# Kernel tuning notes

Measured on AMD Instinct MI355X. Metric: run time of the kernel, lower is better.

## Reference

```python
import jax, jax.numpy as jnp
import numpy as np

N = 4096          # num_nodes == batch (every node sampled once)
D_EMB = 512       # n_embd (temporal encoder width)
D_GNN = 256       # gnn_embd
H = 2             # num_heads (hardcoded in GraphAttentionLayer default)
D_HEAD = D_GNN // H
FUS = D_EMB + D_GNN
EDGE_P = 32.0 / N # avg degree ~ max_neighbors
ALPHA = 0.2
NEG_INF = -9e15


def layer_norm(x, g, b, eps=1e-5):
    m = jnp.mean(x, axis=-1, keepdims=True)
    v = jnp.var(x, axis=-1, keepdims=True)
    return (x - m) / jnp.sqrt(v + eps) * g + b


def setup_inputs() -> dict:
    key = jax.random.key(0)
    ks = jax.random.split(key, 12)
    s = lambda fan: 1.0 / np.sqrt(fan)
    h_temporal = jax.random.normal(ks[0], (N, D_EMB), jnp.float32)
    node_indices = jnp.arange(N, dtype=jnp.int32)
    adj = (jax.random.uniform(ks[1], (N, N)) < EDGE_P).astype(jnp.float32)
    adj = jnp.maximum(adj, jnp.eye(N, dtype=jnp.float32))  # self-loops
    W_proj = jax.random.normal(ks[2], (D_EMB, D_GNN), jnp.float32) * s(D_EMB)
    b_proj = jnp.zeros((D_GNN,), jnp.float32)
    W_gat = jax.random.normal(ks[3], (H, D_GNN, D_HEAD), jnp.float32) * s(D_GNN)
    a_gat = jax.random.normal(ks[4], (H, 2 * D_HEAD), jnp.float32) * s(2 * D_HEAD)
    node_emb = jax.random.normal(ks[5], (N, D_GNN), jnp.float32) * 0.02
    ln_g = jnp.ones((D_GNN,), jnp.float32)
    ln_b = jnp.zeros((D_GNN,), jnp.float32)
    ln2_g = jnp.ones((FUS,), jnp.float32)
    ln2_b = jnp.zeros((FUS,), jnp.float32)
    W1 = jax.random.normal(ks[6], (FUS, FUS // 2), jnp.float32) * s(FUS)
    b1 = jnp.zeros((FUS // 2,), jnp.float32)
    W2 = jax.random.normal(ks[7], (FUS // 2, 1), jnp.float32) * s(FUS // 2)
    b2 = jnp.zeros((1,), jnp.float32)
    return dict(h_temporal=h_temporal, node_indices=node_indices, adj=adj,
                W_proj=W_proj, b_proj=b_proj, W_gat=W_gat, a_gat=a_gat,
                node_emb=node_emb, ln_g=ln_g, ln_b=ln_b,
                ln2_g=ln2_g, ln2_b=ln2_b, W1=W1, b1=b1, W2=W2, b2=b2)


def reference(h_temporal, node_indices, adj, W_proj, b_proj, W_gat, a_gat,
              node_emb, ln_g, ln_b, ln2_g, ln2_b, W1, b1, W2, b2):
    # gnn_proj
    h_gnn_in = h_temporal @ W_proj + b_proj                     # (B, D_GNN)
    # scatter-mean of batch features onto graph nodes (torch.unique + index_add_)
    counts = jax.ops.segment_sum(jnp.ones((h_gnn_in.shape[0],), h_gnn_in.dtype),
                                 node_indices, num_segments=N)
    sums = jax.ops.segment_sum(h_gnn_in, node_indices, num_segments=N)
    uniq_feats = sums / jnp.clip(counts, 1.0)[:, None]
    # nodes present in batch use averaged temporal feats, others keep learned embedding
    sub_feats = jnp.where((counts > 0)[:, None], uniq_feats, node_emb)  # (N, D_GNN)
    # multi-head GAT: e[h,i,j] = leakyrelu(a1_h . Wh_i + a2_h . Wh_j)
    Wh = jnp.einsum('ni,hid->hnd', sub_feats, W_gat)            # (H, N, d)
    f_src = jnp.einsum('hnd,hd->hn', Wh, a_gat[:, :D_HEAD])     # query half
    f_dst = jnp.einsum('hnd,hd->hn', Wh, a_gat[:, D_HEAD:])     # key half
    e = jax.nn.leaky_relu(f_src[:, :, None] + f_dst[:, None, :], ALPHA)  # (H,N,N)
    e = jnp.where(adj[None] > 0, e, NEG_INF)
    att = jax.nn.softmax(e, axis=-1)                            # softmax over neighbors j
    hp = jnp.einsum('hnm,hmd->hnd', att, Wh)                    # (H, N, d)
    hp = jnp.transpose(hp, (1, 0, 2)).reshape(N, D_GNN)         # concat heads
    hp = jax.nn.elu(hp)                                         # concat=True
    sub_out = layer_norm(hp, ln_g, ln_b)
    h_graph = sub_out[node_indices]                             # gather back to batch
    # fusion head
    hc = jnp.concatenate([h_temporal, h_graph], axis=-1)        # (B, FUS)
    z = layer_norm(hc, ln2_g, ln2_b)
    z = jax.nn.gelu(z @ W1 + b1, approximate=False)
    out = z @ W2 + b2                                           # (B, 1)
    return out
```

## Files before the change

kernel.cpp:

```cpp
#include <hip/hip_runtime.h>
#include <hip/hip_bf16.h>
#include <math.h>

#define N_NODES 4096
#define D_EMB   512
#define D_GNN   256
#define D_HEAD  128
#define FUS     768
#define D_HID   384
#define MAX_NBR 512

typedef unsigned short u16;
typedef __attribute__((ext_vector_type(4))) float f4;
typedef __attribute__((ext_vector_type(4))) int   i4;
typedef __attribute__((address_space(3))) u16 lds_u16;
typedef __attribute__((address_space(1))) const u16 g_u16;

__device__ __forceinline__ u16 bfh(float x) {
    __hip_bfloat16 b = __float2bfloat16(x);
    return *(u16*)&b;
}
__device__ __forceinline__ float bff(u16 u) {
    __hip_bfloat16 b = *(__hip_bfloat16*)&u;
    return __bfloat162float(b);
}

#define MFMA(acc, a, b) \
    asm volatile("v_mfma_f32_16x16x32_bf16 %0, %1, %2, %0" : "+v"(acc) : "v"(a), "v"(b))

__device__ __forceinline__ float block_reduce(float v, float* red, bool is_max) {
    #pragma unroll
    for (int o = 32; o; o >>= 1)
        v = is_max ? fmaxf(v, __shfl_down(v, o)) : v + __shfl_down(v, o);
    const int wid = threadIdx.x >> 6;
    if ((threadIdx.x & 63) == 0) red[wid] = v;
    __syncthreads();
    float r;
    if (is_max) r = fmaxf(fmaxf(red[0], red[1]), fmaxf(red[2], red[3]));
    else        r = red[0] + red[1] + red[2] + red[3];
    __syncthreads();
    return r;
}

__global__ __launch_bounds__(256) void split_rm(const float* __restrict__ X,
                                                u16* __restrict__ H, u16* __restrict__ L,
                                                int n4) {
    const int i = blockIdx.x * 256 + threadIdx.x;
    if (i >= n4) return;
    const float4 v = ((const float4*)X)[i];
    ushort4 h, l;
    h.x = bfh(v.x); l.x = bfh(v.x - bff(h.x));
    h.y = bfh(v.y); l.y = bfh(v.y - bff(h.y));
    h.z = bfh(v.z); l.z = bfh(v.z - bff(h.z));
    h.w = bfh(v.w); l.w = bfh(v.w - bff(h.w));
    ((ushort4*)H)[i] = h;
    ((ushort4*)L)[i] = l;
}

__device__ __forceinline__ void split_t_body(const float* __restrict__ W,
                                             u16* __restrict__ Th, u16* __restrict__ Tl,
                                             int K, int Nn, int bx, int by,
                                             float (*tile)[33]) {
    const int k0 = by * 32, n0 = bx * 32;
    const int lx = threadIdx.x & 31, ly = threadIdx.x >> 5;
    #pragma unroll
    for (int r = ly; r < 32; r += 8)
        tile[r][lx] = W[(size_t)(k0 + r) * Nn + n0 + lx];
    __syncthreads();
    #pragma unroll
    for (int r = ly; r < 32; r += 8) {
        const float v = tile[lx][r];
        const u16 h = bfh(v);
        const size_t o = (size_t)(n0 + r) * K + k0 + lx;
        Th[o] = h;
        Tl[o] = bfh(v - bff(h));
    }
}

__global__ __launch_bounds__(256) void prep_w(const float* __restrict__ Wproj,
                                              const float* __restrict__ W1,
                                              const float* __restrict__ Wgat,
                                              u16* __restrict__ WpTh, u16* __restrict__ WpTl,
                                              u16* __restrict__ W1Th, u16* __restrict__ W1Tl,
                                              u16* __restrict__ bTh,  u16* __restrict__ bTl) {
    __shared__ float tile[32][33];
    const int b = blockIdx.x;
    if (b < 128) {
        split_t_body(Wproj, WpTh, WpTl, D_EMB, D_GNN, b & 7, b >> 3, tile);
    } else if (b < 416) {
        const int i = b - 128;
        split_t_body(W1, W1Th, W1Tl, FUS, D_HID, i % 12, i / 12, tile);
    } else {
        const int i = b - 416;
        const int n = threadIdx.x;
        const int h = n >> 7, d = n & 127;
        const float v = Wgat[(size_t)h * D_GNN * D_HEAD + (size_t)i * D_HEAD + d];
        const u16 hh = bfh(v);
        bTh[(size_t)n * D_GNN + i] = hh;
        bTl[(size_t)n * D_GNN + i] = bfh(v - bff(hh));
    }
}

template<int SPLIT>
__global__ __launch_bounds__(256) void mgemm(const u16* __restrict__ Ah, const u16* __restrict__ Al,
                                             const u16* __restrict__ Bh, const u16* __restrict__ Bl,
                                             float* __restrict__ C,
                                             int M, int Nn, int K) {
    __shared__ u16 lds[2][4][4096];
    const int t = threadIdx.x, w = t >> 6, l = t & 63;
    const int m0 = blockIdx.y * 64, n0 = blockIdx.x * 64;
    const int nk_per = (K >> 6) / SPLIT;
    const int kt0 = blockIdx.z * nk_per;
    float* Cz = C + (size_t)blockIdx.z * M * Nn;
    const u16* pAh = Ah + (size_t)(m0 + (t >> 3)) * K + (t & 7) * 8;
    const u16* pAl = Al + (size_t)(m0 + (t >> 3)) * K + (t & 7) * 8;
    const u16* pBh = Bh + (size_t)(n0 + (t >> 3)) * K + (t & 7) * 8;
    const u16* pBl = Bl + (size_t)(n0 + (t >> 3)) * K + (t & 7) * 8;
    const int w512 = w * 512;
    const int K32 = K * 32;

#define STG(c, koff) do { \
    __builtin_amdgcn_global_load_lds((g_u16*)(pAh + (koff)),       (lds_u16*)&lds[c][0][w512],        16, 0, 0); \
    __builtin_amdgcn_global_load_lds((g_u16*)(pAh + (koff) + K32), (lds_u16*)&lds[c][0][w512 + 2048], 16, 0, 0); \
    __builtin_amdgcn_global_load_lds((g_u16*)(pAl + (koff)),       (lds_u16*)&lds[c][1][w512],        16, 0, 0); \
    __builtin_amdgcn_global_load_lds((g_u16*)(pAl + (koff) + K32), (lds_u16*)&lds[c][1][w512 + 2048], 16, 0, 0); \
    __builtin_amdgcn_global_load_lds((g_u16*)(pBh + (koff)),       (lds_u16*)&lds[c][2][w512],        16, 0, 0); \
    __builtin_amdgcn_global_load_lds((g_u16*)(pBh + (koff) + K32), (lds_u16*)&lds[c][2][w512 + 2048], 16, 0, 0); \
    __builtin_amdgcn_global_load_lds((g_u16*)(pBl + (koff)),       (lds_u16*)&lds[c][3][w512],        16, 0, 0); \
    __builtin_amdgcn_global_load_lds((g_u16*)(pBl + (koff) + K32), (lds_u16*)&lds[c][3][w512 + 2048], 16, 0, 0); \
} while (0)

    const int wm = w >> 1, wn = w & 1;
    const int lr = l & 15, lk = (l >> 4) << 3;
    int aoff[2][2], boff[2][2];
    #pragma unroll
    for (int i = 0; i < 2; ++i)
        #pragma unroll
        for (int ks = 0; ks < 2; ++ks) {
            aoff[i][ks] = (wm * 32 + i * 16 + lr) * 64 + ks * 32 + lk;
            boff[i][ks] = (wn * 32 + i * 16 + lr) * 64 + ks * 32 + lk;
        }

    f4 acc[2][2] = {};
    int cur = 0;
    STG(0, kt0 * 64);
    __syncthreads();
    for (int kt = kt0; kt < kt0 + nk_per; ++kt) {
        if (kt + 1 < kt0 + nk_per) STG(cur ^ 1, (kt + 1) * 64);
        const u16* LAh = lds[cur][0];
        const u16* LAl = lds[cur][1];
        const u16* LBh = lds[cur][2];
        const u16* LBl = lds[cur][3];
        i4 ah[2][2], al_[2][2], bh[2][2], bl_[2][2];
        #pragma unroll
        for (int i = 0; i < 2; ++i)
            #pragma unroll
            for (int ks = 0; ks < 2; ++ks) {
                ah[i][ks]  = *(const i4*)&LAh[aoff[i][ks]];
                al_[i][ks] = *(const i4*)&LAl[aoff[i][ks]];
                bh[i][ks]  = *(const i4*)&LBh[boff[i][ks]];
                bl_[i][ks] = *(const i4*)&LBl[boff[i][ks]];
            }
        #pragma unroll
        for (int i = 0; i < 2; ++i)
            #pragma unroll
            for (int j = 0; j < 2; ++j)
                #pragma unroll
                for (int ks = 0; ks < 2; ++ks) {
                    MFMA(acc[i][j], ah[i][ks],  bh[j][ks]);
                    MFMA(acc[i][j], ah[i][ks],  bl_[j][ks]);
                    MFMA(acc[i][j], al_[i][ks], bh[j][ks]);
                }
        __syncthreads();
        cur ^= 1;
    }
    asm volatile("s_nop 7\n\ts_nop 7\n\ts_nop 7");
    #pragma unroll
    for (int i = 0; i < 2; ++i)
        #pragma unroll
        for (int j = 0; j < 2; ++j) {
            const int col = n0 + wn * 32 + j * 16 + lr;
            #pragma unroll
            for (int r = 0; r < 4; ++r) {
                const int row = m0 + wm * 32 + i * 16 + (l >> 4) * 4 + r;
                Cz[(size_t)row * Nn + col] = acc[i][j][r];
            }
        }
#undef STG
}

template<bool GELU, bool HASB>
__global__ __launch_bounds__(256) void redk(const float* __restrict__ A,
                                            const float* __restrict__ B,
                                            const float* __restrict__ bias,
                                            float* __restrict__ C,
                                            int n4, int nb4) {
    const int i = blockIdx.x * 256 + threadIdx.x;
    if (i >= n4) return;
    const float4 a = ((const float4*)A)[i];
    const float4 b = ((const float4*)B)[i];
    float4 c = make_float4(a.x + b.x, a.y + b.y, a.z + b.z, a.w + b.w);
    if (HASB) {
        const float4 bv = ((const float4*)bias)[i % nb4];
        c.x += bv.x; c.y += bv.y; c.z += bv.z; c.w += bv.w;
    }
    if (GELU) {
        c.x = 0.5f * c.x * (1.f + erff(c.x * 0.70710678118654752f));
        c.y = 0.5f * c.y * (1.f + erff(c.y * 0.70710678118654752f));
        c.z = 0.5f * c.z * (1.f + erff(c.z * 0.70710678118654752f));
        c.w = 0.5f * c.w * (1.f + erff(c.w * 0.70710678118654752f));
    }
    ((float4*)C)[i] = c;
}

__global__ __launch_bounds__(256) void scatter_add(const float* __restrict__ hgnn,
                                                   const int* __restrict__ nidx,
                                                   float* __restrict__ sums,
                                                   float* __restrict__ counts) {
    const int b = blockIdx.x, t = threadIdx.x;
    const int g = nidx[b];
    atomicAdd(&sums[(size_t)g * D_GNN + t], hgnn[(size_t)b * D_GNN + t]);
    if (t == 0) atomicAdd(&counts[g], 1.0f);
}

__global__ __launch_bounds__(256) void combine(const float* __restrict__ sums,
                                               const float* __restrict__ counts,
                                               const float* __restrict__ nemb,
                                               u16* __restrict__ subh,
                                               u16* __restrict__ subl) {
    const int n = blockIdx.x, t = threadIdx.x;
    const float c = counts[n];
    const size_t o = (size_t)n * D_GNN + t;
    const float v = (c > 0.f) ? sums[o] / fmaxf(c, 1.f) : nemb[o];
    const u16 h = bfh(v);
    subh[o] = h;
    subl[o] = bfh(v - bff(h));
}

__global__ __launch_bounds__(256) void fsd(const float* __restrict__ Wh,
                                           const float* __restrict__ agat,
                                           float* __restrict__ fsrc,
                                           float* __restrict__ fdst) {
    const int n = blockIdx.x * 4 + (threadIdx.x >> 6);
    const int l = threadIdx.x & 63;
    const float* row = Wh + (size_t)n * D_GNN;
    const float x0 = row[l],       x1 = row[l + 64];
    const float y0 = row[128 + l], y1 = row[192 + l];
    float s0 = x0 * agat[l]       + x1 * agat[l + 64];
    float s1 = x0 * agat[128 + l] + x1 * agat[192 + l];
    float s2 = y0 * agat[256 + l] + y1 * agat[320 + l];
    float s3 = y0 * agat[384 + l] + y1 * agat[448 + l];
    #pragma unroll
    for (int o = 32; o; o >>= 1) {
        s0 += __shfl_down(s0, o); s1 += __shfl_down(s1, o);
        s2 += __shfl_down(s2, o); s3 += __shfl_down(s3, o);
    }
    if (l == 0) {
        fsrc[n] = s0;            fdst[n] = s1;
        fsrc[N_NODES + n] = s2;  fdst[N_NODES + n] = s3;
    }
}

__global__ __launch_bounds__(256) void gat_attn(const float* __restrict__ adj,
                                                const float* __restrict__ Wh,
                                                const float* __restrict__ fsrc,
                                                const float* __restrict__ fdst,
                                                const float* __restrict__ lng,
                                                const float* __restrict__ lnb,
                                                float* __restrict__ subout) {
    const int i = blockIdx.x, t = threadIdx.x;
    const int lane = t & 63, wid = t >> 6;
    __shared__ int   s_nbr[MAX_NBR];
    __shared__ int   s_wsum[4];
    __shared__ float s_att[2][MAX_NBR];
    __shared__ float s_red[4];
    __shared__ float s_inv[2];

    const float4* arow4 = (const float4*)(adj + (size_t)i * N_NODES) + t * 4;
    const float4 c0 = arow4[0], c1 = arow4[1], c2 = arow4[2], c3 = arow4[3];
    float v[16];
    *(float4*)&v[0]  = c0; *(float4*)&v[4]  = c1;
    *(float4*)&v[8]  = c2; *(float4*)&v[12] = c3;
    int mask = 0;
    #pragma unroll
    for (int k = 0; k < 16; ++k) mask |= (v[k] > 0.f) ? (1 << k) : 0;
    const int cnt_t = __popc(mask);

    int pre = cnt_t;
    #pragma unroll
    for (int o = 1; o < 64; o <<= 1) {
        const int u = __shfl_up(pre, o);
        if (lane >= o) pre += u;
    }
    if (lane == 63) s_wsum[wid] = pre;
    __syncthreads();
    int base = 0;
    for (int w = 0; w < wid; ++w) base += s_wsum[w];
    const int total = s_wsum[0] + s_wsum[1] + s_wsum[2] + s_wsum[3];
    int off = base + pre - cnt_t;
    #pragma unroll
    for (int k = 0; k < 16; ++k)
        if ((mask >> k) & 1) {
            if (off < MAX_NBR) s_nbr[off] = t * 16 + k;
            ++off;
        }
    __syncthreads();
    const int cnt = min(total, MAX_NBR);

    for (int h = 0; h < 2; ++h) {
        const float fs = fsrc[h * N_NODES + i];
        const float* fd = fdst + h * N_NODES;
        float lm = -1e30f;
        for (int idx = t; idx < cnt; idx += 256) {
            float e = fs + fd[s_nbr[idx]];
            e = e > 0.f ? e : 0.2f * e;
            s_att[h][idx] = e;
            lm = fmaxf(lm, e);
        }
        const float m = block_reduce(lm, s_red, true);
        float ls = 0.f;
        for (int idx = t; idx < cnt; idx += 256) {
            const float p = expf(s_att[h][idx] - m);
            s_att[h][idx] = p;
            ls += p;
        }
        const float s = block_reduce(ls, s_red, false);
        if (t == 0) s_inv[h] = 1.f / s;
    }
    __syncthreads();

    const int h = t >> 7, d = t & 127;
    float acc = 0.f;
    for (int j = 0; j < cnt; ++j)
        acc += s_att[h][j] * Wh[(size_t)s_nbr[j] * D_GNN + h * D_HEAD + d];
    acc *= s_inv[h];
    const float vv = acc > 0.f ? acc : expm1f(acc);
    const float sum  = block_reduce(vv, s_red, false);
    const float sq   = block_reduce(vv * vv, s_red, false);
    const float mean = sum * (1.f / 256.f);
    const float var  = sq * (1.f / 256.f) - mean * mean;
    const float rstd = rsqrtf(var + 1e-5f);
    subout[(size_t)i * D_GNN + t] = (vv - mean) * rstd * lng[t] + lnb[t];
}

__global__ __launch_bounds__(256) void fuse_ln(const float* __restrict__ ht,
                                               const float* __restrict__ subout,
                                               const int* __restrict__ nidx,
                                               const float* __restrict__ g,
                                               const float* __restrict__ b,
                                               u16* __restrict__ znh,
                                               u16* __restrict__ znl) {
    const int row = blockIdx.x, t = threadIdx.x;
    __shared__ float s_red[4];
    const int gidx = nidx[row];
    const float x0 = ht[(size_t)row * D_EMB + t];
    const float x1 = ht[(size_t)row * D_EMB + 256 + t];
    const float x2 = subout[(size_t)gidx * D_GNN + t];
    const float sum = block_reduce(x0 + x1 + x2, s_red, false);
    const float sq  = block_reduce(x0 * x0 + x1 * x1 + x2 * x2, s_red, false);
    const float mean = sum * (1.f / 768.f);
    const float var  = sq * (1.f / 768.f) - mean * mean;
    const float rstd = rsqrtf(var + 1e-5f);
    const size_t base = (size_t)row * FUS;
    const float z0 = (x0 - mean) * rstd * g[t]       + b[t];
    const float z1 = (x1 - mean) * rstd * g[256 + t] + b[256 + t];
    const float z2 = (x2 - mean) * rstd * g[512 + t] + b[512 + t];
    u16 h;
    h = bfh(z0); znh[base + t]       = h; znl[base + t]       = bfh(z0 - bff(h));
    h = bfh(z1); znh[base + 256 + t] = h; znl[base + 256 + t] = bfh(z1 - bff(h));
    h = bfh(z2); znh[base + 512 + t] = h; znl[base + 512 + t] = bfh(z2 - bff(h));
}

__global__ __launch_bounds__(256) void outk(const float* __restrict__ z1,
                                            const float* __restrict__ W2,
                                            const float* __restrict__ b2,
                                            float* __restrict__ out) {
    const int row = blockIdx.x * 4 + (threadIdx.x >> 6);
    const int l = threadIdx.x & 63;
    float acc = 0.f;
    for (int c = l; c < D_HID; c += 64)
        acc += z1[(size_t)row * D_HID + c] * W2[c];
    #pragma unroll
    for (int o = 32; o; o >>= 1) acc += __shfl_down(acc, o);
    if (l == 0) out[row] = acc + b2[0];
}

extern "C" void kernel_launch(void* const* d_in, const int* in_sizes, int n_in,
                              void* d_out, int out_size, void* d_ws, size_t ws_size,
                              hipStream_t stream) {
    const float* ht    = (const float*)d_in[0];
    const int*   nidx  = (const int*)  d_in[1];
    const float* adj   = (const float*)d_in[2];
    const float* Wproj = (const float*)d_in[3];
    const float* bproj = (const float*)d_in[4];
    const float* Wgat  = (const float*)d_in[5];
    const float* agat  = (const float*)d_in[6];
    const float* nemb  = (const float*)d_in[7];
    const float* lng   = (const float*)d_in[8];
    const float* lnb   = (const float*)d_in[9];
    const float* ln2g  = (const float*)d_in[10];
    const float* ln2b  = (const float*)d_in[11];
    const float* W1    = (const float*)d_in[12];
    const float* b1    = (const float*)d_in[13];
    const float* W2    = (const float*)d_in[14];
    const float* b2    = (const float*)d_in[15];
    float* out = (float*)d_out;

    float* f_sums = (float*)d_ws;
    float* f_cnt  = f_sums + 1048576;
    float* g1     = f_cnt  + 4096;
    float* f_hgnn = g1     + 2097152;
    float* g2     = f_hgnn + 1048576;
    float* f_wh   = g2     + 2097152;
    float* g3     = f_wh   + 1048576;
    float* f_z1   = g3     + 3145728;
    float* f_fsrc = f_z1   + 1572864;
    float* f_fdst = f_fsrc + 8192;
    float* f_subo = f_fdst + 8192;
    u16*   ht_hi  = (u16*)(f_subo + 1048576);
    u16*   ht_lo  = ht_hi  + 2097152;
    u16*   subf_h = ht_lo  + 2097152;
    u16*   subf_l = subf_h + 1048576;
    u16*   zn_hi  = subf_l + 1048576;
    u16*   zn_lo  = zn_hi  + 3145728;
    u16*   WpT_h  = zn_lo  + 3145728;
    u16*   WpT_l  = WpT_h  + 131072;
    u16*   bT_h   = WpT_l  + 131072;
    u16*   bT_l   = bT_h   + 65536;
    u16*   W1T_h  = bT_l   + 65536;
    u16*   W1T_l  = W1T_h  + 294912;

    hipMemsetAsync(f_sums, 0, (1048576 + 4096) * sizeof(float), stream);

    prep_w<<<672, 256, 0, stream>>>(Wproj, W1, Wgat, WpT_h, WpT_l, W1T_h, W1T_l, bT_h, bT_l);
    split_rm<<<2048, 256, 0, stream>>>(ht, ht_hi, ht_lo, 524288);
    mgemm<2><<<dim3(4, 64, 2), 256, 0, stream>>>(
        ht_hi, ht_lo, WpT_h, WpT_l, g1, N_NODES, D_GNN, D_EMB);
    redk<false, true><<<1024, 256, 0, stream>>>(g1, g1 + 1048576, bproj, f_hgnn, 262144, 64);
    scatter_add<<<N_NODES, 256, 0, stream>>>(f_hgnn, nidx, f_sums, f_cnt);
    combine<<<N_NODES, 256, 0, stream>>>(f_sums, f_cnt, nemb, subf_h, subf_l);
    mgemm<2><<<dim3(4, 64, 2), 256, 0, stream>>>(
        subf_h, subf_l, bT_h, bT_l, g2, N_NODES, D_GNN, D_GNN);
    redk<false, false><<<1024, 256, 0, stream>>>(g2, g2 + 1048576, nullptr, f_wh, 262144, 64);
    fsd<<<N_NODES / 4, 256, 0, stream>>>(f_wh, agat, f_fsrc, f_fdst);
    gat_attn<<<N_NODES, 256, 0, stream>>>(adj, f_wh, f_fsrc, f_fdst, lng, lnb, f_subo);
    fuse_ln<<<N_NODES, 256, 0, stream>>>(ht, f_subo, nidx, ln2g, ln2b, zn_hi, zn_lo);
    mgemm<2><<<dim3(6, 64, 2), 256, 0, stream>>>(
        zn_hi, zn_lo, W1T_h, W1T_l, g3, N_NODES, D_HID, FUS);
    redk<true, true><<<1536, 256, 0, stream>>>(g3, g3 + 1572864, b1, f_z1, 393216, 96);
    outk<<<N_NODES / 4, 256, 0, stream>>>(f_z1, W2, b2, out);
}
```

Baseline: 223.5 us.

## Fuse GEMM epilogues, triple-buffer LDS with swizzle, unroll GAT neighbor aggregation

Drops the split-K GEMM and its separate reduction kernels. Bias and GELU are now applied in the GEMM epilogue, which removes three launches and the round trips of the partial sums through memory. The GEMM mainloop moves to a three-stage LDS pipeline with explicit vmcnt waits and an XOR swizzle on the LDS layout to reduce bank conflicts. The GAT neighbour aggregation loop is unrolled by four with independent accumulators to expose memory-level parallelism. Without split-K the GEMMs launch half as many blocks (256 and 384), which risks lower occupancy, and the larger LDS footprint may limit resident blocks per CU.

```diff
diff --git a/kernel.cpp b/kernel.cpp
--- a/kernel.cpp
+++ b/kernel.cpp
@@ -101,21 +101,21 @@
     }
 }
 
-template<int SPLIT>
+template<bool GELU, bool HASB>
 __global__ __launch_bounds__(256) void mgemm(const u16* __restrict__ Ah, const u16* __restrict__ Al,
                                              const u16* __restrict__ Bh, const u16* __restrict__ Bl,
-                                             float* __restrict__ C,
+                                             const float* __restrict__ bias, float* __restrict__ C,
                                              int M, int Nn, int K) {
-    __shared__ u16 lds[2][4][4096];
+    __shared__ u16 lds[3][4][4096];
     const int t = threadIdx.x, w = t >> 6, l = t & 63;
     const int m0 = blockIdx.y * 64, n0 = blockIdx.x * 64;
-    const int nk_per = (K >> 6) / SPLIT;
-    const int kt0 = blockIdx.z * nk_per;
-    float* Cz = C + (size_t)blockIdx.z * M * Nn;
-    const u16* pAh = Ah + (size_t)(m0 + (t >> 3)) * K + (t & 7) * 8;
-    const u16* pAl = Al + (size_t)(m0 + (t >> 3)) * K + (t & 7) * 8;
-    const u16* pBh = Bh + (size_t)(n0 + (t >> 3)) * K + (t & 7) * 8;
-    const u16* pBl = Bl + (size_t)(n0 + (t >> 3)) * K + (t & 7) * 8;
+    const int nk = K >> 6;
+    const int r8 = t >> 3;
+    const int c8 = (t & 7) ^ (r8 & 7);
+    const u16* pAh = Ah + (size_t)(m0 + r8) * K + c8 * 8;
+    const u16* pAl = Al + (size_t)(m0 + r8) * K + c8 * 8;
+    const u16* pBh = Bh + (size_t)(n0 + r8) * K + c8 * 8;
+    const u16* pBl = Bl + (size_t)(n0 + r8) * K + c8 * 8;
     const int w512 = w * 512;
     const int K32 = K * 32;
 
@@ -131,22 +131,36 @@
 } while (0)
 
     const int wm = w >> 1, wn = w & 1;
-    const int lr = l & 15, lk = (l >> 4) << 3;
+    const int lr = l & 15;
+    const int kq = l >> 4;
     int aoff[2][2], boff[2][2];
     #pragma unroll
     for (int i = 0; i < 2; ++i)
         #pragma unroll
         for (int ks = 0; ks < 2; ++ks) {
-            aoff[i][ks] = (wm * 32 + i * 16 + lr) * 64 + ks * 32 + lk;
-            boff[i][ks] = (wn * 32 + i * 16 + lr) * 64 + ks * 32 + lk;
+            const int ar = wm * 32 + i * 16 + lr;
+            const int br = wn * 32 + i * 16 + lr;
+            aoff[i][ks] = ar * 64 + (((ks << 2) + kq) ^ (ar & 7)) * 8;
+            boff[i][ks] = br * 64 + (((ks << 2) + kq) ^ (br & 7)) * 8;
         }
 
     f4 acc[2][2] = {};
+    STG(0, 0);
+    if (nk > 1) STG(1, 64);
     int cur = 0;
-    STG(0, kt0 * 64);
-    __syncthreads();
-    for (int kt = kt0; kt < kt0 + nk_per; ++kt) {
-        if (kt + 1 < kt0 + nk_per) STG(cur ^ 1, (kt + 1) * 64);
+    for (int kt = 0; kt < nk; ++kt) {
+        const int ahead = nk - 1 - kt;
+        if (ahead >= 2) {
+            const int nxt2 = (cur >= 1) ? cur - 1 : 2;
+            STG(nxt2, (kt + 2) * 64);
+            asm volatile("s_waitcnt vmcnt(16)" ::: "memory");
+        } else if (ahead == 1) {
+            asm volatile("s_waitcnt vmcnt(8)" ::: "memory");
+        } else {
+            asm volatile("s_waitcnt vmcnt(0)" ::: "memory");
+        }
+        __builtin_amdgcn_s_barrier();
+        __builtin_amdgcn_sched_barrier(0);
         const u16* LAh = lds[cur][0];
         const u16* LAl = lds[cur][1];
         const u16* LBh = lds[cur][2];
@@ -171,8 +185,9 @@
                     MFMA(acc[i][j], ah[i][ks],  bl_[j][ks]);
                     MFMA(acc[i][j], al_[i][ks], bh[j][ks]);
                 }
-        __syncthreads();
-        cur ^= 1;
+        __builtin_amdgcn_sched_barrier(0);
+        __builtin_amdgcn_s_barrier();
+        cur = (cur == 2) ? 0 : cur + 1;
     }
     asm volatile("s_nop 7\n\ts_nop 7\n\ts_nop 7");
     #pragma unroll
@@ -180,37 +195,17 @@
         #pragma unroll
         for (int j = 0; j < 2; ++j) {
             const int col = n0 + wn * 32 + j * 16 + lr;
+            float bv = 0.f;
+            if (HASB) bv = bias[col];
             #pragma unroll
             for (int r = 0; r < 4; ++r) {
                 const int row = m0 + wm * 32 + i * 16 + (l >> 4) * 4 + r;
-                Cz[(size_t)row * Nn + col] = acc[i][j][r];
+                float v = acc[i][j][r] + bv;
+                if (GELU) v = 0.5f * v * (1.f + erff(v * 0.70710678118654752f));
+                C[(size_t)row * Nn + col] = v;
             }
         }
 #undef STG
-}
-
-template<bool GELU, bool HASB>
-__global__ __launch_bounds__(256) void redk(const float* __restrict__ A,
-                                            const float* __restrict__ B,
-                                            const float* __restrict__ bias,
-                                            float* __restrict__ C,
-                                            int n4, int nb4) {
-    const int i = blockIdx.x * 256 + threadIdx.x;
-    if (i >= n4) return;
-    const float4 a = ((const float4*)A)[i];
-    const float4 b = ((const float4*)B)[i];
-    float4 c = make_float4(a.x + b.x, a.y + b.y, a.z + b.z, a.w + b.w);
-    if (HASB) {
-        const float4 bv = ((const float4*)bias)[i % nb4];
-        c.x += bv.x; c.y += bv.y; c.z += bv.z; c.w += bv.w;
-    }
-    if (GELU) {
-        c.x = 0.5f * c.x * (1.f + erff(c.x * 0.70710678118654752f));
-        c.y = 0.5f * c.y * (1.f + erff(c.y * 0.70710678118654752f));
-        c.z = 0.5f * c.z * (1.f + erff(c.z * 0.70710678118654752f));
-        c.w = 0.5f * c.w * (1.f + erff(c.w * 0.70710678118654752f));
-    }
-    ((float4*)C)[i] = c;
 }
 
 __global__ __launch_bounds__(256) void scatter_add(const float* __restrict__ hgnn,
@@ -330,10 +325,20 @@
     __syncthreads();
 
     const int h = t >> 7, d = t & 127;
-    float acc = 0.f;
-    for (int j = 0; j < cnt; ++j)
-        acc += s_att[h][j] * Wh[(size_t)s_nbr[j] * D_GNN + h * D_HEAD + d];
-    acc *= s_inv[h];
+    const float* att = s_att[h];
+    const int hd = h * D_HEAD + d;
+    float a0 = 0.f, a1 = 0.f, a2 = 0.f, a3 = 0.f;
+    int j = 0;
+    for (; j + 4 <= cnt; j += 4) {
+        a0 += att[j]     * Wh[(size_t)s_nbr[j]     * D_GNN + hd];
+        a1 += att[j + 1] * Wh[(size_t)s_nbr[j + 1] * D_GNN + hd];
+        a2 += att[j + 2] * Wh[(size_t)s_nbr[j + 2] * D_GNN + hd];
+        a3 += att[j + 3] * Wh[(size_t)s_nbr[j + 3] * D_GNN + hd];
+    }
+    for (; j < cnt; ++j)
+        a0 += att[j] * Wh[(size_t)s_nbr[j] * D_GNN + hd];
+    float acc = ((a0 + a1) + (a2 + a3)) * s_inv[h];
+
     const float vv = acc > 0.f ? acc : expm1f(acc);
     const float sum  = block_reduce(vv, s_red, false);
     const float sq   = block_reduce(vv * vv, s_red, false);
@@ -408,12 +413,9 @@
 
     float* f_sums = (float*)d_ws;
     float* f_cnt  = f_sums + 1048576;
-    float* g1     = f_cnt  + 4096;
-    float* f_hgnn = g1     + 2097152;
-    float* g2     = f_hgnn + 1048576;
-    float* f_wh   = g2     + 2097152;
-    float* g3     = f_wh   + 1048576;
-    float* f_z1   = g3     + 3145728;
+    float* f_hgnn = f_cnt  + 4096;
+    float* f_wh   = f_hgnn + 1048576;
+    float* f_z1   = f_wh   + 1048576;
     float* f_fsrc = f_z1   + 1572864;
     float* f_fdst = f_fsrc + 8192;
     float* f_subo = f_fdst + 8192;
@@ -434,19 +436,16 @@
 
     prep_w<<<672, 256, 0, stream>>>(Wproj, W1, Wgat, WpT_h, WpT_l, W1T_h, W1T_l, bT_h, bT_l);
     split_rm<<<2048, 256, 0, stream>>>(ht, ht_hi, ht_lo, 524288);
-    mgemm<2><<<dim3(4, 64, 2), 256, 0, stream>>>(
-        ht_hi, ht_lo, WpT_h, WpT_l, g1, N_NODES, D_GNN, D_EMB);
-    redk<false, true><<<1024, 256, 0, stream>>>(g1, g1 + 1048576, bproj, f_hgnn, 262144, 64);
+    mgemm<false, true><<<dim3(4, 64), 256, 0, stream>>>(
+        ht_hi, ht_lo, WpT_h, WpT_l, bproj, f_hgnn, N_NODES, D_GNN, D_EMB);
     scatter_add<<<N_NODES, 256, 0, stream>>>(f_hgnn, nidx, f_sums, f_cnt);
     combine<<<N_NODES, 256, 0, stream>>>(f_sums, f_cnt, nemb, subf_h, subf_l);
-    mgemm<2><<<dim3(4, 64, 2), 256, 0, stream>>>(
-        subf_h, subf_l, bT_h, bT_l, g2, N_NODES, D_GNN, D_GNN);
-    redk<false, false><<<1024, 256, 0, stream>>>(g2, g2 + 1048576, nullptr, f_wh, 262144, 64);
+    mgemm<false, false><<<dim3(4, 64), 256, 0, stream>>>(
+        subf_h, subf_l, bT_h, bT_l, nullptr, f_wh, N_NODES, D_GNN, D_GNN);
     fsd<<<N_NODES / 4, 256, 0, stream>>>(f_wh, agat, f_fsrc, f_fdst);
     gat_attn<<<N_NODES, 256, 0, stream>>>(adj, f_wh, f_fsrc, f_fdst, lng, lnb, f_subo);
     fuse_ln<<<N_NODES, 256, 0, stream>>>(ht, f_subo, nidx, ln2g, ln2b, zn_hi, zn_lo);
-    mgemm<2><<<dim3(6, 64, 2), 256, 0, stream>>>(
-        zn_hi, zn_lo, W1T_h, W1T_l, g3, N_NODES, D_HID, FUS);
-    redk<true, true><<<1536, 256, 0, stream>>>(g3, g3 + 1572864, b1, f_z1, 393216, 96);
+    mgemm<true, true><<<dim3(6, 64), 256, 0, stream>>>(
+        zn_hi, zn_lo, W1T_h, W1T_l, b1, f_z1, N_NODES, D_HID, FUS);
     outk<<<N_NODES / 4, 256, 0, stream>>>(f_z1, W2, b2, out);
 }
```

Measured after the change: 215.1 us. 1.04x faster.
